# Performance work log

Measured on AMD Instinct MI355X. Metric: run time of the kernel, lower is better.

The kernel has to match this reference:

```python
import jax, jax.numpy as jnp
import numpy as np

BETA = 0.25
EPS = 1e-12

def setup_inputs() -> dict:
    key = jax.random.key(0)
    k1, k2 = jax.random.split(key)
    f_BChw = jax.random.normal(k1, (32, 64, 32, 32), dtype=jnp.float32)
    emb_weight = jax.random.normal(k2, (8192, 64), dtype=jnp.float32)
    return {"f_BChw": f_BChw, "emb_weight": emb_weight}

def reference(f_BChw, emb_weight):
    f = f_BChw.astype(jnp.float32)
    B, C, h, w = f.shape
    V = emb_weight.shape[0]
    # flatten tokens: [B,C,h,w] -> [N,C]
    NxC = jnp.transpose(f, (0, 2, 3, 1)).reshape(-1, C)
    # cosine nearest-neighbor on detached, L2-normalized queries/codes
    q = jax.lax.stop_gradient(NxC)
    q = q / jnp.maximum(jnp.linalg.norm(q, axis=-1, keepdims=True), EPS)
    wn = emb_weight / jnp.maximum(jnp.linalg.norm(emb_weight, axis=-1, keepdims=True), EPS)
    sim = q @ wn.T                      # [N,V] -- dominant memory traffic
    idx_N = jnp.argmax(sim, axis=1)     # [N]
    # gather codes -> [B,C,h,w]
    fhat = emb_weight[idx_N].reshape(B, h, w, C).transpose(0, 3, 1, 2)
    sg = jax.lax.stop_gradient
    vq_loss = BETA * jnp.mean((sg(fhat) - f) ** 2) + jnp.mean((fhat - sg(f)) ** 2)
    # straight-through estimator
    fhat_out = f + sg(fhat - f)
    # usage statistics (bincount)
    counts = jnp.zeros((V,), jnp.float32).at[idx_N].add(1.0)
    prob = counts / counts.sum()
    vocab_usage = jnp.mean((prob > 0.01 / V).astype(jnp.float32)) * 100.0
    entropy_loss = jnp.float32(0.0)
    return fhat_out, vq_loss, entropy_loss, vocab_usage
```

## Files before the change

### kernel.cpp

```cpp
#include <hip/hip_runtime.h>

typedef _Float16 f16x8 __attribute__((ext_vector_type(8)));
typedef float f32x16 __attribute__((ext_vector_type(16)));

#define V_TOTAL 8192
#define C_DIM   64
#define N_TOK   32768
#define VSPLIT  4
#define VSEG    (V_TOTAL / VSPLIT)
#define CHUNKS  (VSEG / 32)
#define INV2048 4.8828125e-4f


__device__ __forceinline__ unsigned long long packkey(float s, int idx) {
    unsigned u = __float_as_uint(s);
    unsigned k = u ^ ((unsigned)(((int)u) >> 31) | 0x80000000u);
    return ((unsigned long long)k << 32) | (unsigned)(8191 - idx);
}

__global__ __launch_bounds__(256)
void k_prep(const float* __restrict__ w, _Float16* __restrict__ cp,
            unsigned long long* __restrict__ keys, int* __restrict__ counts) {
    int v = blockIdx.x * 256 + threadIdx.x;
    counts[v] = 0;
#pragma unroll
    for (int i = 0; i < 4; ++i) keys[v * 4 + i] = 0ull;
    const float4* row = (const float4*)(w + v * C_DIM);
    float4 r[16];
    float s = 0.f;
#pragma unroll
    for (int i = 0; i < 16; ++i) {
        r[i] = row[i];
        s += r[i].x * r[i].x + r[i].y * r[i].y + r[i].z * r[i].z + r[i].w * r[i].w;
    }
    float inv = 1.0f / fmaxf(sqrtf(s), 1e-12f);
    const float* rs = (const float*)r;
    const int cv = v >> 5, c = v & 31;
#pragma unroll
    for (int q = 0; q < 8; ++q) {
        f16x8 hi, lo;
#pragma unroll
        for (int j = 0; j < 8; ++j) {
            float x = rs[q * 8 + j] * inv;
            _Float16 h = (_Float16)x;
            hi[j] = h;
            lo[j] = (_Float16)((x - (float)h) * 2048.0f);
        }
        *(f16x8*)(cp + cv * 4096 +        q * 256 + c * 8) = hi;
        *(f16x8*)(cp + cv * 4096 + 2048 + q * 256 + c * 8) = lo;
    }
}

__global__ __launch_bounds__(64, 2)
void k_argmax(const float* __restrict__ f, const _Float16* __restrict__ cp,
              unsigned long long* __restrict__ keys) {
    const int lane = threadIdx.x;
    const int c31  = lane & 31;
    const int g    = lane >> 5;
    const int seg  = blockIdx.y;
    const int t0   = blockIdx.x * 64;

    f16x8 bh[2][4], bl[2][4];
#pragma unroll
    for (int tg = 0; tg < 2; ++tg) {
        const int T = t0 + tg * 32 + c31;
        const float* fb = f + (T >> 10) * 65536 + (T & 1023);
#pragma unroll
        for (int ks = 0; ks < 4; ++ks) {
#pragma unroll
            for (int j = 0; j < 8; ++j) {
                float v = fb[(ks * 16 + g * 8 + j) * 1024];
                _Float16 h = (_Float16)v;
                bh[tg][ks][j] = h;
                bl[tg][ks][j] = (_Float16)((v - (float)h) * 2048.0f);
            }
        }
    }

    const _Float16* cA = cp + seg * (CHUNKS * 4096) + g * 256 + c31 * 8;

    f32x16 zacc = {0.f,0.f,0.f,0.f,0.f,0.f,0.f,0.f,0.f,0.f,0.f,0.f,0.f,0.f,0.f,0.f};

    float best0 = -3.4e38f, best1 = -3.4e38f;
    int   bidx0 = 0,        bidx1 = 0;

    f16x8 AHa[4], ALa[4], AHb[4], ALb[4];

    auto ldchunk = [&](f16x8 (&AH)[4], f16x8 (&AL)[4], int cv) {
#pragma unroll
        for (int ks = 0; ks < 4; ++ks) {
            AH[ks] = *(const f16x8*)(cA + cv * 4096 + ks * 512);
            AL[ks] = *(const f16x8*)(cA + cv * 4096 + 2048 + ks * 512);
        }
    };

    auto compute = [&](const f16x8 (&AH)[4], const f16x8 (&AL)[4], int cv) {
        f32x16 a00, a01, a10, a11;
        a00 = __builtin_amdgcn_mfma_f32_32x32x16_f16(AH[0], bh[0][0], zacc, 0, 0, 0);
        a01 = __builtin_amdgcn_mfma_f32_32x32x16_f16(AH[0], bl[0][0], zacc, 0, 0, 0);
        a10 = __builtin_amdgcn_mfma_f32_32x32x16_f16(AH[0], bh[1][0], zacc, 0, 0, 0);
        a11 = __builtin_amdgcn_mfma_f32_32x32x16_f16(AH[0], bl[1][0], zacc, 0, 0, 0);
        a01 = __builtin_amdgcn_mfma_f32_32x32x16_f16(AL[0], bh[0][0], a01, 0, 0, 0);
        a11 = __builtin_amdgcn_mfma_f32_32x32x16_f16(AL[0], bh[1][0], a11, 0, 0, 0);
#pragma unroll
        for (int ks = 1; ks < 4; ++ks) {
            a00 = __builtin_amdgcn_mfma_f32_32x32x16_f16(AH[ks], bh[0][ks], a00, 0, 0, 0);
            a01 = __builtin_amdgcn_mfma_f32_32x32x16_f16(AH[ks], bl[0][ks], a01, 0, 0, 0);
            a10 = __builtin_amdgcn_mfma_f32_32x32x16_f16(AH[ks], bh[1][ks], a10, 0, 0, 0);
            a11 = __builtin_amdgcn_mfma_f32_32x32x16_f16(AH[ks], bl[1][ks], a11, 0, 0, 0);
            a01 = __builtin_amdgcn_mfma_f32_32x32x16_f16(AL[ks], bh[0][ks], a01, 0, 0, 0);
            a11 = __builtin_amdgcn_mfma_f32_32x32x16_f16(AL[ks], bh[1][ks], a11, 0, 0, 0);
        }
        const int codebase = seg * VSEG + cv * 32;
#pragma unroll
        for (int r = 0; r < 16; ++r) {
            const int codeq = codebase + (r & 3) + 8 * (r >> 2);
            float s0 = fmaf(a01[r], INV2048, a00[r]);
            bool u0 = s0 > best0;
            best0 = u0 ? s0 : best0;
            bidx0 = u0 ? codeq : bidx0;
            float s1 = fmaf(a11[r], INV2048, a10[r]);
            bool u1 = s1 > best1;
            best1 = u1 ? s1 : best1;
            bidx1 = u1 ? codeq : bidx1;
        }
    };

    ldchunk(AHa, ALa, 0);
    for (int cv = 0; cv < CHUNKS; cv += 2) {
        ldchunk(AHb, ALb, cv + 1);
        compute(AHa, ALa, cv);
        if (cv + 2 < CHUNKS) ldchunk(AHa, ALa, cv + 2);
        compute(AHb, ALb, cv + 1);
    }

    bidx0 += 4 * g;
    bidx1 += 4 * g;
    {
        float ov = __shfl_xor(best0, 32);
        int   oi = __shfl_xor(bidx0, 32);
        if (ov > best0 || (ov == best0 && oi < bidx0)) { best0 = ov; bidx0 = oi; }
        ov = __shfl_xor(best1, 32);
        oi = __shfl_xor(bidx1, 32);
        if (ov > best1 || (ov == best1 && oi < bidx1)) { best1 = ov; bidx1 = oi; }
    }
    if (lane < 32) {
        atomicMax(&keys[t0 + c31],      packkey(best0, bidx0));
        atomicMax(&keys[t0 + 32 + c31], packkey(best1, bidx1));
    }
}

__global__ __launch_bounds__(256)
void k_finalize(const float* __restrict__ f, const float* __restrict__ w,
                const unsigned long long* __restrict__ keys,
                int* __restrict__ counts, float* __restrict__ blocksq,
                float* __restrict__ out) {
    const int tid = threadIdx.x;
    const int t   = blockIdx.x * 256 + tid;

    const int bi = 8191 - (int)(unsigned)(keys[t] & 0xFFFFFFFFull);
    atomicAdd(&counts[bi], 1);

    float4 cr[16];
    const float4* crow = (const float4*)(w + bi * C_DIM);
#pragma unroll
    for (int i = 0; i < 16; ++i) cr[i] = crow[i];
    const float* crs = (const float*)cr;

    const int bb = t >> 10;
    const int hw = t & 1023;
    const float* fb = f + bb * 65536 + hw;
    float*       ob = out + bb * 65536 + hw;

    float s = 0.f;
#pragma unroll
    for (int c = 0; c < C_DIM; ++c) {
        float fv = fb[c * 1024];
        float fh = crs[c];
        float d  = fh - fv;
        s += d * d;
        ob[c * 1024] = fv + d;
    }

    __shared__ float red[256];
    red[tid] = s;
    __syncthreads();
    for (int st = 128; st > 0; st >>= 1) {
        if (tid < st) red[tid] += red[tid + st];
        __syncthreads();
    }
    if (tid == 0) blocksq[blockIdx.x] = red[0];
}

__global__ __launch_bounds__(256)
void k_stats(const int* __restrict__ counts, const float* __restrict__ blocksq,
             float* __restrict__ out) {
    __shared__ float redf[256];
    __shared__ int   redi[256];
    const int tid = threadIdx.x;
    int used = 0;
    for (int v = tid; v < V_TOTAL; v += 256) used += (counts[v] > 0) ? 1 : 0;
    redi[tid] = used;
    redf[tid] = (tid < 128) ? blocksq[tid] : 0.f;
    __syncthreads();
    for (int st = 128; st > 0; st >>= 1) {
        if (tid < st) { redi[tid] += redi[tid + st]; redf[tid] += redf[tid + st]; }
        __syncthreads();
    }
    if (tid == 0) {
        float mse = redf[0] / 2097152.0f;
        out[2097152] = 0.25f * mse + mse;
        out[2097153] = 0.0f;
        out[2097154] = 100.0f * (float)redi[0] / 8192.0f;
    }
}

extern "C" void kernel_launch(void* const* d_in, const int* in_sizes, int n_in,
                              void* d_out, int out_size, void* d_ws, size_t ws_size,
                              hipStream_t stream) {
    const float* f = (const float*)d_in[0];
    const float* w = (const float*)d_in[1];
    float* out = (float*)d_out;
    float* ws  = (float*)d_ws;

    _Float16*           cp      = (_Float16*)ws;
    unsigned long long* keys    = (unsigned long long*)(ws + 524288);
    int*                counts  = (int*)(ws + 589824);
    float*              blocksq = ws + 598016;

    hipLaunchKernelGGL(k_prep, dim3(32), dim3(256), 0, stream, w, cp, keys, counts);
    hipLaunchKernelGGL(k_argmax, dim3(512, VSPLIT), dim3(64), 0, stream,
                       f, cp, keys);
    hipLaunchKernelGGL(k_finalize, dim3(128), dim3(256), 0, stream,
                       f, w, keys, counts, blocksq, out);
    hipLaunchKernelGGL(k_stats, dim3(1), dim3(256), 0, stream,
                       counts, blocksq, out);
}
```

Baseline: 126.4 us.

## Share codebook chunks across four waves via LDS with async global-to-LDS loads

The argmax kernel becomes a 256-thread block of four waves, each handling 32 tokens. The block stages each 32-code chunk of the codebook into double-buffered LDS with global_load_lds, so one copy is shared by all waves instead of every wave reading it from global memory into registers. Each wave now does one 32-token tile with three MFMAs per k-step instead of two tiles. This cuts global and L2 traffic for codebook reads, but adds a block-wide barrier per chunk and halves the MFMA work each wave has to hide latency.

```diff
diff --git a/kernel.cpp b/kernel.cpp
--- a/kernel.cpp
+++ b/kernel.cpp
@@ -11,6 +11,9 @@
 #define CHUNKS  (VSEG / 32)
 #define INV2048 4.8828125e-4f
 
+typedef const __attribute__((address_space(1))) _Float16 glb_f16;
+typedef __attribute__((address_space(3))) _Float16 lds_f16;
+
 
 __device__ __forceinline__ unsigned long long packkey(float s, int idx) {
     unsigned u = __float_as_uint(s);
@@ -51,19 +54,22 @@
     }
 }
 
-__global__ __launch_bounds__(64, 2)
+__global__ __launch_bounds__(256, 4)
 void k_argmax(const float* __restrict__ f, const _Float16* __restrict__ cp,
               unsigned long long* __restrict__ keys) {
-    const int lane = threadIdx.x;
+    __shared__ __align__(16) _Float16 lds[2][4096];
+
+    const int tid  = threadIdx.x;
+    const int lane = tid & 63;
+    const int wid  = tid >> 6;
     const int c31  = lane & 31;
     const int g    = lane >> 5;
     const int seg  = blockIdx.y;
-    const int t0   = blockIdx.x * 64;
-
-    f16x8 bh[2][4], bl[2][4];
-#pragma unroll
-    for (int tg = 0; tg < 2; ++tg) {
-        const int T = t0 + tg * 32 + c31;
+    const int t0   = blockIdx.x * 128 + wid * 32;
+
+    f16x8 bh[4], bl[4];
+    {
+        const int T = t0 + c31;
         const float* fb = f + (T >> 10) * 65536 + (T & 1023);
 #pragma unroll
         for (int ks = 0; ks < 4; ++ks) {
@@ -71,82 +77,65 @@
             for (int j = 0; j < 8; ++j) {
                 float v = fb[(ks * 16 + g * 8 + j) * 1024];
                 _Float16 h = (_Float16)v;
-                bh[tg][ks][j] = h;
-                bl[tg][ks][j] = (_Float16)((v - (float)h) * 2048.0f);
+                bh[ks][j] = h;
+                bl[ks][j] = (_Float16)((v - (float)h) * 2048.0f);
             }
         }
     }
 
-    const _Float16* cA = cp + seg * (CHUNKS * 4096) + g * 256 + c31 * 8;
-
-    f32x16 zacc = {0.f,0.f,0.f,0.f,0.f,0.f,0.f,0.f,0.f,0.f,0.f,0.f,0.f,0.f,0.f,0.f};
-
-    float best0 = -3.4e38f, best1 = -3.4e38f;
-    int   bidx0 = 0,        bidx1 = 0;
-
-    f16x8 AHa[4], ALa[4], AHb[4], ALb[4];
-
-    auto ldchunk = [&](f16x8 (&AH)[4], f16x8 (&AL)[4], int cv) {
+    const _Float16* seg_cp = cp + (size_t)seg * (CHUNKS * 4096);
+
+    auto stage = [&](int cv, int buf) {
+        const _Float16* src = seg_cp + cv * 4096 + wid * 1024 + lane * 8;
+        _Float16* dst = &lds[buf][wid * 1024];
+        __builtin_amdgcn_global_load_lds((glb_f16*)src,       (lds_f16*)dst,       16, 0, 0);
+        __builtin_amdgcn_global_load_lds((glb_f16*)(src+512), (lds_f16*)(dst+512), 16, 0, 0);
+    };
+
+    f32x16 am = {0.f,0.f,0.f,0.f,0.f,0.f,0.f,0.f,0.f,0.f,0.f,0.f,0.f,0.f,0.f,0.f};
+    f32x16 ac = am;
+
+    float best = -3.4e38f;
+    int   bidx = 0;
+
+    stage(0, 0);
+    __syncthreads();
+
+    for (int cv = 0; cv < CHUNKS; ++cv) {
+        if (cv + 1 < CHUNKS) stage(cv + 1, (cv + 1) & 1);
+
+        const _Float16* base = &lds[cv & 1][g * 256 + c31 * 8];
 #pragma unroll
         for (int ks = 0; ks < 4; ++ks) {
-            AH[ks] = *(const f16x8*)(cA + cv * 4096 + ks * 512);
-            AL[ks] = *(const f16x8*)(cA + cv * 4096 + 2048 + ks * 512);
-        }
-    };
-
-    auto compute = [&](const f16x8 (&AH)[4], const f16x8 (&AL)[4], int cv) {
-        f32x16 a00, a01, a10, a11;
-        a00 = __builtin_amdgcn_mfma_f32_32x32x16_f16(AH[0], bh[0][0], zacc, 0, 0, 0);
-        a01 = __builtin_amdgcn_mfma_f32_32x32x16_f16(AH[0], bl[0][0], zacc, 0, 0, 0);
-        a10 = __builtin_amdgcn_mfma_f32_32x32x16_f16(AH[0], bh[1][0], zacc, 0, 0, 0);
-        a11 = __builtin_amdgcn_mfma_f32_32x32x16_f16(AH[0], bl[1][0], zacc, 0, 0, 0);
-        a01 = __builtin_amdgcn_mfma_f32_32x32x16_f16(AL[0], bh[0][0], a01, 0, 0, 0);
-        a11 = __builtin_amdgcn_mfma_f32_32x32x16_f16(AL[0], bh[1][0], a11, 0, 0, 0);
-#pragma unroll
-        for (int ks = 1; ks < 4; ++ks) {
-            a00 = __builtin_amdgcn_mfma_f32_32x32x16_f16(AH[ks], bh[0][ks], a00, 0, 0, 0);
-            a01 = __builtin_amdgcn_mfma_f32_32x32x16_f16(AH[ks], bl[0][ks], a01, 0, 0, 0);
-            a10 = __builtin_amdgcn_mfma_f32_32x32x16_f16(AH[ks], bh[1][ks], a10, 0, 0, 0);
-            a11 = __builtin_amdgcn_mfma_f32_32x32x16_f16(AH[ks], bl[1][ks], a11, 0, 0, 0);
-            a01 = __builtin_amdgcn_mfma_f32_32x32x16_f16(AL[ks], bh[0][ks], a01, 0, 0, 0);
-            a11 = __builtin_amdgcn_mfma_f32_32x32x16_f16(AL[ks], bh[1][ks], a11, 0, 0, 0);
-        }
+            f16x8 AH = *(const f16x8*)(base + ks * 512);
+            f16x8 AL = *(const f16x8*)(base + 2048 + ks * 512);
+            am = __builtin_amdgcn_mfma_f32_32x32x16_f16(AH, bh[ks], am, 0, 0, 0);
+            ac = __builtin_amdgcn_mfma_f32_32x32x16_f16(AH, bl[ks], ac, 0, 0, 0);
+            ac = __builtin_amdgcn_mfma_f32_32x32x16_f16(AL, bh[ks], ac, 0, 0, 0);
+        }
+
         const int codebase = seg * VSEG + cv * 32;
 #pragma unroll
         for (int r = 0; r < 16; ++r) {
             const int codeq = codebase + (r & 3) + 8 * (r >> 2);
-            float s0 = fmaf(a01[r], INV2048, a00[r]);
-            bool u0 = s0 > best0;
-            best0 = u0 ? s0 : best0;
-            bidx0 = u0 ? codeq : bidx0;
-            float s1 = fmaf(a11[r], INV2048, a10[r]);
-            bool u1 = s1 > best1;
-            best1 = u1 ? s1 : best1;
-            bidx1 = u1 ? codeq : bidx1;
-        }
-    };
-
-    ldchunk(AHa, ALa, 0);
-    for (int cv = 0; cv < CHUNKS; cv += 2) {
-        ldchunk(AHb, ALb, cv + 1);
-        compute(AHa, ALa, cv);
-        if (cv + 2 < CHUNKS) ldchunk(AHa, ALa, cv + 2);
-        compute(AHb, ALb, cv + 1);
-    }
-
-    bidx0 += 4 * g;
-    bidx1 += 4 * g;
+            float s = fmaf(ac[r], INV2048, am[r]);
+            bool u = s > best;
+            best = u ? s : best;
+            bidx = u ? codeq : bidx;
+            am[r] = 0.f;
+            ac[r] = 0.f;
+        }
+        __syncthreads();
+    }
+
+    bidx += 4 * g;
     {
-        float ov = __shfl_xor(best0, 32);
-        int   oi = __shfl_xor(bidx0, 32);
-        if (ov > best0 || (ov == best0 && oi < bidx0)) { best0 = ov; bidx0 = oi; }
-        ov = __shfl_xor(best1, 32);
-        oi = __shfl_xor(bidx1, 32);
-        if (ov > best1 || (ov == best1 && oi < bidx1)) { best1 = ov; bidx1 = oi; }
+        float ov = __shfl_xor(best, 32);
+        int   oi = __shfl_xor(bidx, 32);
+        if (ov > best || (ov == best && oi < bidx)) { best = ov; bidx = oi; }
     }
     if (lane < 32) {
-        atomicMax(&keys[t0 + c31],      packkey(best0, bidx0));
-        atomicMax(&keys[t0 + 32 + c31], packkey(best1, bidx1));
+        atomicMax(&keys[t0 + c31], packkey(best, bidx));
     }
 }
 
@@ -229,7 +218,7 @@
     float*              blocksq = ws + 598016;
 
     hipLaunchKernelGGL(k_prep, dim3(32), dim3(256), 0, stream, w, cp, keys, counts);
-    hipLaunchKernelGGL(k_argmax, dim3(512, VSPLIT), dim3(64), 0, stream,
+    hipLaunchKernelGGL(k_argmax, dim3(N_TOK / 128, VSPLIT), dim3(256), 0, stream,
                        f, cp, keys);
     hipLaunchKernelGGL(k_finalize, dim3(128), dim3(256), 0, stream,
                        f, w, keys, counts, blocksq, out);
```

Measured after the change: 123.4 us. -2.4%, faster.
